# Performance work log

Measured on AMD Instinct MI355X. Metric: run time of the kernel, lower is better.

## Reference

```python
import jax, jax.numpy as jnp
import numpy as np

D_MODEL = 1024
NUM_HEADS = 16
D_K = D_MODEL // NUM_HEADS


def setup_inputs() -> dict:
    key = jax.random.key(0)
    ks = jax.random.split(key, 11)
    B, S = 2, 2048
    scale = 1.0 / np.sqrt(D_MODEL)
    inp = {
        'q': jax.random.normal(ks[0], (B, S, D_MODEL), dtype=jnp.float32),
        'k': jax.random.normal(ks[1], (B, S, D_MODEL), dtype=jnp.float32),
        'v': jax.random.normal(ks[2], (B, S, D_MODEL), dtype=jnp.float32),
        'W_q': jax.random.normal(ks[3], (D_MODEL, D_MODEL), dtype=jnp.float32) * scale,
        'b_q': jnp.zeros((D_MODEL,), dtype=jnp.float32),
        'W_k': jax.random.normal(ks[4], (D_MODEL, D_MODEL), dtype=jnp.float32) * scale,
        'b_k': jnp.zeros((D_MODEL,), dtype=jnp.float32),
        'W_v': jax.random.normal(ks[5], (D_MODEL, D_MODEL), dtype=jnp.float32) * scale,
        'b_v': jnp.zeros((D_MODEL,), dtype=jnp.float32),
        'W_o': jax.random.normal(ks[6], (D_MODEL, D_MODEL), dtype=jnp.float32) * scale,
        'b_o': jnp.zeros((D_MODEL,), dtype=jnp.float32),
    }
    return inp


def _split_heads(x):
    # [B, S, D] -> [B, H, S, d_k]
    B, S, _ = x.shape
    return x.reshape(B, S, NUM_HEADS, D_K).transpose(0, 2, 1, 3)


def reference(q, k, v, W_q, b_q, W_k, b_k, W_v, b_v, W_o, b_o):
    # Linear projections (torch Linear: x @ W.T + b)
    qh = _split_heads(q @ W_q.T + b_q)  # [B,H,S,dk]
    kh = _split_heads(k @ W_k.T + b_k)
    vh = _split_heads(v @ W_v.T + b_v)
    scores = jnp.einsum('bhsd,bhtd->bhst', qh, kh) / jnp.sqrt(
        jnp.asarray(D_K, dtype=qh.dtype))  # [B,H,S,S]
    probs = jax.nn.softmax(scores, axis=-1)
    attn = jnp.einsum('bhst,bhtd->bhsd', probs, vh)  # [B,H,S,dk]
    B, H, S, dk = attn.shape
    combined = attn.transpose(0, 2, 1, 3).reshape(B, S, H * dk)  # [B,S,D]
    return combined @ W_o.T + b_o
```

## Files before the change

### kernel.cpp

```cpp
#include <hip/hip_runtime.h>
#include <hip/hip_bf16.h>

typedef __bf16 bf16;
typedef __attribute__((ext_vector_type(4))) __bf16 bf16x4;
typedef __attribute__((ext_vector_type(8))) __bf16 bf16x8;
typedef __attribute__((ext_vector_type(4))) float f32x4;
typedef __attribute__((ext_vector_type(4))) short short4v;

#define AS1C(p) ((const __attribute__((address_space(1))) void*)(p))
#define AS3(p)  ((__attribute__((address_space(3))) void*)(p))

static constexpr int B_ = 2, S_ = 2048, DM = 1024, H_ = 16, DK = 64;
static constexpr int M_ = B_ * S_;
static constexpr int NW = DM * DM;
static constexpr float QSCL = 0.125f * 1.44269504088896340736f;

__device__ __forceinline__ float fast_exp2(float x) {
#if __has_builtin(__builtin_amdgcn_exp2f)
  return __builtin_amdgcn_exp2f(x);
#else
  return exp2f(x);
#endif
}

__device__ __forceinline__ f32x4 mfma_pv(bf16x4 a, bf16x4 b, f32x4 c) {
#if __has_builtin(__builtin_amdgcn_mfma_f32_16x16x16_bf16)
  return __builtin_amdgcn_mfma_f32_16x16x16_bf16(a, b, c, 0, 0, 0);
#else
  union U { bf16x4 h; short4v s; };
  U ua; ua.h = a;
  U ub; ub.h = b;
  return __builtin_amdgcn_mfma_f32_16x16x16bf16_1k(ua.s, ub.s, c, 0, 0, 0);
#endif
}

__device__ __forceinline__ int vperm_tok(int tok) {
  const int t5 = tok & 31;
  return (tok & ~31) | (((t5 >> 2) & 3) * 8) | (((t5 >> 4) & 1) * 4);
}

__global__ __launch_bounds__(256) void cast_all(
    const float* Wq, const float* Wk, const float* Wv, const float* Wo,
    const float* q, const float* k, const float* v,
    bf16* Wc, bf16* WoC, bf16* qc, bf16* kc, bf16* vc)
{
  const int id = blockIdx.x;
  const float* in;
  bf16* out;
  float s = 1.0f;
  int base;
  if (id < 2048) {
    const int z = id >> 9;
    base = id & 511;
    in  = z == 0 ? Wq : (z == 1 ? Wk : (z == 2 ? Wv : Wo));
    out = z < 3 ? (Wc + (size_t)z * NW) : WoC;
    if (z == 0) s = QSCL;
  } else {
    const int z = (id - 2048) >> 11;
    base = (id - 2048) & 2047;
    in  = z == 0 ? q : (z == 1 ? k : v);
    out = z == 0 ? qc : (z == 1 ? kc : vc);
  }
  const size_t i = ((size_t)base * 256 + threadIdx.x) * 8;
  f32x4 a = *(const f32x4*)(in + i);
  f32x4 b2 = *(const f32x4*)(in + i + 4);
  bf16x8 o;
#pragma unroll
  for (int j = 0; j < 4; ++j) { o[j] = (bf16)(a[j] * s); o[4 + j] = (bf16)(b2[j] * s); }
  *(bf16x8*)(out + i) = o;
}

__global__ __launch_bounds__(256, 3) void gemm_qkv_b(
    const bf16* __restrict__ qc, const bf16* __restrict__ kc,
    const bf16* __restrict__ vc, const bf16* __restrict__ Wc,
    const float* b0, const float* b1, const float* b2,
    bf16* C0, bf16* C1, bf16* C2, int M, int N, int K)
{
  const int id = blockIdx.x;
  const int z  = id >> 8;
  const int r  = id & 255;
  const int by = r & 31;
  const int bx = r >> 5;
  const bf16* A = z == 0 ? qc : (z == 1 ? kc : vc);
  const float* bias = z == 0 ? b0 : (z == 1 ? b1 : b2);
  const float bscale = z == 0 ? QSCL : 1.0f;
  const bf16* W = Wc + (size_t)z * NW;
  bf16* Cout = z == 0 ? C0 : (z == 1 ? C1 : C2);
  const bool transv = (z == 2);

  __shared__ bf16 As[2 * 128 * 32];
  __shared__ bf16 Bs[2 * 128 * 32];

  const int tid  = threadIdx.x;
  const int wave = tid >> 6, lane = tid & 63;
  const int quad = lane >> 4, l16 = lane & 15;
  const int wm = wave >> 1, wn = wave & 1;
  const int row0 = by * 128;
  const int col0 = bx * 128;

  const int srow  = lane >> 2;
  const int skcol = (lane & 3) * 8;

  f32x4 acc[4][4] = {};

  for (int k0 = 0; k0 < K; k0 += 64) {
    __syncthreads();
#pragma unroll
    for (int hf = 0; hf < 2; ++hf)
#pragma unroll
      for (int c = wave; c < 8; c += 4)
        __builtin_amdgcn_global_load_lds(
            AS1C(A + (size_t)(row0 + c * 16 + srow) * K + k0 + hf * 32 + skcol),
            AS3(As + hf * 4096 + c * 512), 16, 0, 0);
#pragma unroll
    for (int hf = 0; hf < 2; ++hf)
#pragma unroll
      for (int i = 0; i < 2; ++i) {
        const int c = wave * 2 + i;
        __builtin_amdgcn_global_load_lds(
            AS1C(W + (size_t)(col0 + c * 16 + srow) * K + k0 + hf * 32 + skcol),
            AS3(Bs + hf * 4096 + c * 512), 16, 0, 0);
      }
    __syncthreads();

#pragma unroll
    for (int hf = 0; hf < 2; ++hf) {
      bf16x8 a[4], bfr[4];
#pragma unroll
      for (int i = 0; i < 4; ++i)
        a[i] = *(const bf16x8*)(As + hf * 4096 + (wm * 64 + i * 16 + l16) * 32 + quad * 8);
#pragma unroll
      for (int j = 0; j < 4; ++j)
        bfr[j] = *(const bf16x8*)(Bs + hf * 4096 + (wn * 64 + j * 16 + l16) * 32 + quad * 8);
#pragma unroll
      for (int i = 0; i < 4; ++i)
#pragma unroll
        for (int j = 0; j < 4; ++j)
          acc[i][j] = __builtin_amdgcn_mfma_f32_16x16x32_bf16(a[i], bfr[j], acc[i][j], 0, 0, 0);
    }
  }

#pragma unroll
  for (int j = 0; j < 4; ++j) {
    const int col = col0 + wn * 64 + j * 16 + l16;
    const float bv = bias[col] * bscale;
    if (transv) {
      const int hh = col >> 6, dd = col & 63;
#pragma unroll
      for (int i = 0; i < 4; ++i) {
        const int row = row0 + wm * 64 + i * 16 + quad * 4;
        const int bb2 = row >> 11, tok = row & 2047;
        const int tokp = vperm_tok(tok);
        bf16x4 o;
#pragma unroll
        for (int r2 = 0; r2 < 4; ++r2) o[r2] = (bf16)(acc[i][j][r2] + bv);
        *(bf16x4*)(Cout + (((size_t)bb2 * H_ + hh) * DK + dd) * S_ + tokp) = o;
      }
    } else {
#pragma unroll
      for (int i = 0; i < 4; ++i)
#pragma unroll
        for (int r2 = 0; r2 < 4; ++r2) {
          const int row = row0 + wm * 64 + i * 16 + quad * 4 + r2;
          Cout[(size_t)row * N + col] = (bf16)(acc[i][j][r2] + bv);
        }
    }
  }
}

__global__ __launch_bounds__(256) void gemm_qkv_f(
    const float* A0, const float* A1, const float* A2,
    const bf16* __restrict__ Wc,
    const float* b0, const float* b1, const float* b2,
    bf16* C0, bf16* C1, bf16* C2, int M, int N, int K)
{
  const int id = blockIdx.x;
  const int z  = id >> 8;
  const int r  = id & 255;
  const int by = r & 31;
  const int bx = r >> 5;
  const float* A = z == 0 ? A0 : (z == 1 ? A1 : A2);
  const float* bias = z == 0 ? b0 : (z == 1 ? b1 : b2);
  const float bscale = z == 0 ? QSCL : 1.0f;
  const bf16* W = Wc + (size_t)z * NW;
  bf16* Cout = z == 0 ? C0 : (z == 1 ? C1 : C2);
  const bool transv = (z == 2);

  __shared__ bf16 As[2 * 128 * 32];
  __shared__ bf16 Bs[2 * 128 * 32];

  const int tid  = threadIdx.x;
  const int wave = tid >> 6, lane = tid & 63;
  const int quad = lane >> 4, l16 = lane & 15;
  const int wm = wave >> 1, wn = wave & 1;
  const int row0 = by * 128;
  const int col0 = bx * 128;

  const int srow  = lane >> 2;
  const int skcol = (lane & 3) * 8;

  const int arow  = (tid >> 1) & 127;
  const int ak16  = (tid & 1) * 16;
  const float* agp = A + (size_t)(row0 + arow) * K + ak16;
  f32x4 pre[8];
#pragma unroll
  for (int hf = 0; hf < 2; ++hf)
#pragma unroll
    for (int c = 0; c < 4; ++c)
      pre[hf * 4 + c] = *(const f32x4*)(agp + hf * 32 + c * 4);

  f32x4 acc[4][4] = {};

  for (int k0 = 0; k0 < K; k0 += 64) {
    __syncthreads();
#pragma unroll
    for (int hf = 0; hf < 2; ++hf) {
      bf16x8 w0, w1;
#pragma unroll
      for (int j = 0; j < 4; ++j) {
        w0[j]     = (bf16)pre[hf * 4 + 0][j];
        w0[4 + j] = (bf16)pre[hf * 4 + 1][j];
        w1[j]     = (bf16)pre[hf * 4 + 2][j];
        w1[4 + j] = (bf16)pre[hf * 4 + 3][j];
      }
      bf16* dst = As + hf * 4096 + arow * 32 + ak16;
      *(bf16x8*)dst = w0;
      *(bf16x8*)(dst + 8) = w1;
    }
#pragma unroll
    for (int hf = 0; hf < 2; ++hf)
#pragma unroll
      for (int i = 0; i < 2; ++i) {
        const int c = wave * 2 + i;
        __builtin_amdgcn_global_load_lds(
            AS1C(W + (size_t)(col0 + c * 16 + srow) * K + k0 + hf * 32 + skcol),
            AS3(Bs + hf * 4096 + c * 512), 16, 0, 0);
      }
    __syncthreads();

    if (k0 + 64 < K) {
#pragma unroll
      for (int hf = 0; hf < 2; ++hf)
#pragma unroll
        for (int c = 0; c < 4; ++c)
          pre[hf * 4 + c] = *(const f32x4*)(agp + k0 + 64 + hf * 32 + c * 4);
    }

#pragma unroll
    for (int hf = 0; hf < 2; ++hf) {
      bf16x8 a[4], bfr[4];
#pragma unroll
      for (int i = 0; i < 4; ++i)
        a[i] = *(const bf16x8*)(As + hf * 4096 + (wm * 64 + i * 16 + l16) * 32 + quad * 8);
#pragma unroll
      for (int j = 0; j < 4; ++j)
        bfr[j] = *(const bf16x8*)(Bs + hf * 4096 + (wn * 64 + j * 16 + l16) * 32 + quad * 8);
#pragma unroll
      for (int i = 0; i < 4; ++i)
#pragma unroll
        for (int j = 0; j < 4; ++j)
          acc[i][j] = __builtin_amdgcn_mfma_f32_16x16x32_bf16(a[i], bfr[j], acc[i][j], 0, 0, 0);
    }
  }

#pragma unroll
  for (int j = 0; j < 4; ++j) {
    const int col = col0 + wn * 64 + j * 16 + l16;
    const float bv = bias[col] * bscale;
    if (transv) {
      const int hh = col >> 6, dd = col & 63;
#pragma unroll
      for (int i = 0; i < 4; ++i) {
        const int row = row0 + wm * 64 + i * 16 + quad * 4;
        const int bb2 = row >> 11, tok = row & 2047;
        const int tokp = vperm_tok(tok);
        bf16x4 o;
#pragma unroll
        for (int r2 = 0; r2 < 4; ++r2) o[r2] = (bf16)(acc[i][j][r2] + bv);
        *(bf16x4*)(Cout + (((size_t)bb2 * H_ + hh) * DK + dd) * S_ + tokp) = o;
      }
    } else {
#pragma unroll
      for (int i = 0; i < 4; ++i)
#pragma unroll
        for (int r2 = 0; r2 < 4; ++r2) {
          const int row = row0 + wm * 64 + i * 16 + quad * 4 + r2;
          Cout[(size_t)row * N + col] = (bf16)(acc[i][j][r2] + bv);
        }
    }
  }
}

__global__ __launch_bounds__(256, 2) void gemm_out(
    const bf16* __restrict__ Ain, const bf16* __restrict__ W,
    const float* __restrict__ bias, float* __restrict__ Cout,
    int M, int N, int K)
{
  const int id = blockIdx.x;
  const int by = id & 63;
  const int bx = id >> 6;

  __shared__ bf16 As0[2 * 64 * 32], As1[2 * 64 * 32];
  __shared__ bf16 Bs0[2 * 128 * 32], Bs1[2 * 128 * 32];

  const int tid  = threadIdx.x;
  const int wave = tid >> 6, lane = tid & 63;
  const int quad = lane >> 4, l16 = lane & 15;
  const int wm = wave >> 1, wn = wave & 1;
  const int row0 = by * 64;
  const int col0 = bx * 128;

  const int srow  = lane >> 2;
  const int skcol = (lane & 3) * 8;

  auto stage_A = [&](int k0, bf16* dst) {
#pragma unroll
    for (int hf = 0; hf < 2; ++hf)
      __builtin_amdgcn_global_load_lds(
          AS1C(Ain + (size_t)(row0 + wave * 16 + srow) * K + k0 + hf * 32 + skcol),
          AS3(dst + hf * 2048 + wave * 512), 16, 0, 0);
  };
  auto stage_W = [&](int k0, bf16* dst) {
#pragma unroll
    for (int hf = 0; hf < 2; ++hf)
#pragma unroll
      for (int i = 0; i < 2; ++i) {
        const int c = wave * 2 + i;
        __builtin_amdgcn_global_load_lds(
            AS1C(W + (size_t)(col0 + c * 16 + srow) * K + k0 + hf * 32 + skcol),
            AS3(dst + hf * 4096 + c * 512), 16, 0, 0);
      }
  };

  f32x4 acc[2][4] = {};

  auto mfma_tile = [&](const bf16* Ab, const bf16* Bb) {
#pragma unroll
    for (int hf = 0; hf < 2; ++hf) {
      bf16x8 a[2], bfr[4];
#pragma unroll
      for (int i = 0; i < 2; ++i)
        a[i] = *(const bf16x8*)(Ab + hf * 2048 + (wm * 32 + i * 16 + l16) * 32 + quad * 8);
#pragma unroll
      for (int j = 0; j < 4; ++j)
        bfr[j] = *(const bf16x8*)(Bb + hf * 4096 + (wn * 64 + j * 16 + l16) * 32 + quad * 8);
#pragma unroll
      for (int i = 0; i < 2; ++i)
#pragma unroll
        for (int j = 0; j < 4; ++j)
          acc[i][j] = __builtin_amdgcn_mfma_f32_16x16x32_bf16(a[i], bfr[j], acc[i][j], 0, 0, 0);
    }
  };

  const int NK = K / 64;
  stage_A(0, As0);
  stage_W(0, Bs0);
  __syncthreads();

  for (int t2 = 0; t2 < NK / 2; ++t2) {
    const int t = t2 * 2;
    if (t + 1 < NK) { stage_A((t + 1) * 64, As1); stage_W((t + 1) * 64, Bs1); }
    mfma_tile(As0, Bs0);
    __syncthreads();
    if (t + 2 < NK) { stage_A((t + 2) * 64, As0); stage_W((t + 2) * 64, Bs0); }
    mfma_tile(As1, Bs1);
    __syncthreads();
  }

#pragma unroll
  for (int j = 0; j < 4; ++j) {
    const int col = col0 + wn * 64 + j * 16 + l16;
    const float bv = bias[col];
#pragma unroll
    for (int i = 0; i < 2; ++i)
#pragma unroll
      for (int r = 0; r < 4; ++r) {
        const int row = row0 + wm * 32 + i * 16 + quad * 4 + r;
        Cout[(size_t)row * N + col] = acc[i][j][r] + bv;
      }
  }
}

__global__ __launch_bounds__(256, 2) void attn_kernel(
    const bf16* Q, const bf16* __restrict__ Kb,
    const bf16* __restrict__ Vtg, bf16* O)
{
  __shared__ bf16 Kt0[64 * 64], Kt1[64 * 64];
  __shared__ bf16 Vt0[64 * 64], Vt1[64 * 64];

  const int tid  = threadIdx.x;
  const int wave = tid >> 6, lane = tid & 63;
  const int quad = lane >> 4, l16 = lane & 15;
  const int id = blockIdx.x;
  const int hb = id & 31;
  const int h = hb & 15, b = hb >> 4;
  const int qt = id >> 5;
  const int qA = qt * 128 + wave * 32;
  const size_t base  = (size_t)b * S_ * DM + (size_t)h * DK;
  const size_t baseV = ((size_t)b * H_ + h) * DK * S_;

  bf16x8 qf[2][2];
#pragma unroll
  for (int f = 0; f < 2; ++f)
#pragma unroll
    for (int kt = 0; kt < 2; ++kt)
      qf[f][kt] = *(const bf16x8*)(Q + base + (size_t)(qA + f * 16 + l16) * DM + kt * 32 + quad * 8);

  const int r8 = lane >> 3;
  const int so = ((lane & 7) ^ r8) << 3;
  const bf16* gK = Kb + base;
  const bf16* gV = Vtg + baseV;

  auto stage = [&](int t, bf16* Kd, bf16* Vd) {
#pragma unroll
    for (int o8 = 0; o8 < 16; o8 += 8) {
      const int row = wave * 16 + o8 + r8;
      __builtin_amdgcn_global_load_lds(
          AS1C(gK + (size_t)(t * 64 + row) * DM + so),
          AS3(Kd + (wave * 16 + o8) * 64), 16, 0, 0);
      __builtin_amdgcn_global_load_lds(
          AS1C(gV + (size_t)row * S_ + t * 64 + so),
          AS3(Vd + (wave * 16 + o8) * 64), 16, 0, 0);
    }
  };

  f32x4 lacc[2] = {};
  f32x4 accO[2][4] = {};
  const int sw = (l16 & 7) << 4;

  auto compute = [&](const bf16* Kc_, const bf16* Vc_) {
    const char* Kc = (const char*)Kc_;
    const char* Vc = (const char*)Vc_;
    f32x4 sc[2][4];
#pragma unroll
    for (int ct = 0; ct < 4; ++ct) {
      const char* kp = Kc + (ct * 16 + l16) * 128;
      const bf16x8 kf0 = *(const bf16x8*)(kp + ((quad * 16) ^ sw));
      const bf16x8 kf1 = *(const bf16x8*)(kp + ((64 + quad * 16) ^ sw));
#pragma unroll
      for (int f = 0; f < 2; ++f) {
        f32x4 a = {0.f, 0.f, 0.f, 0.f};
        a = __builtin_amdgcn_mfma_f32_16x16x32_bf16(kf0, qf[f][0], a, 0, 0, 0);
        a = __builtin_amdgcn_mfma_f32_16x16x32_bf16(kf1, qf[f][1], a, 0, 0, 0);
        sc[f][ct] = a;
      }
    }
    bf16x4 pk[2][4];
#pragma unroll
    for (int f = 0; f < 2; ++f)
#pragma unroll
      for (int ct = 0; ct < 4; ++ct)
#pragma unroll
        for (int r = 0; r < 4; ++r) {
          const float p = fast_exp2(sc[f][ct][r]);
          lacc[f][r] += p;
          pk[f][ct][r] = (bf16)p;
        }
#pragma unroll
    for (int dt = 0; dt < 4; ++dt) {
      const char* vp = Vc + (dt * 16 + l16) * 128;
#pragma unroll
      for (int g = 0; g < 2; ++g) {
        const bf16x8 v8 = *(const bf16x8*)(vp + ((g * 64 + quad * 16) ^ sw));
        const bf16x4 vlo = __builtin_shufflevector(v8, v8, 0, 1, 2, 3);
        const bf16x4 vhi = __builtin_shufflevector(v8, v8, 4, 5, 6, 7);
#pragma unroll
        for (int f = 0; f < 2; ++f) {
          accO[f][dt] = mfma_pv(vlo, pk[f][2 * g],     accO[f][dt]);
          accO[f][dt] = mfma_pv(vhi, pk[f][2 * g + 1], accO[f][dt]);
        }
      }
    }
  };

  constexpr int NIT = S_ / 64;
  stage(0, Kt0, Vt0);
  __syncthreads();

  for (int it = 0; it < NIT; it += 2) {
    if (it + 1 < NIT) stage(it + 1, Kt1, Vt1);
    compute(Kt0, Vt0);
    __syncthreads();
    if (it + 2 < NIT) stage(it + 2, Kt0, Vt0);
    compute(Kt1, Vt1);
    __syncthreads();
  }

#pragma unroll
  for (int f = 0; f < 2; ++f) {
    float l_s = (lacc[f][0] + lacc[f][1]) + (lacc[f][2] + lacc[f][3]);
    l_s += __shfl_xor(l_s, 16, 64);
    l_s += __shfl_xor(l_s, 32, 64);
    const float inv = 1.0f / l_s;
#pragma unroll
    for (int dt = 0; dt < 4; ++dt) {
      bf16x4 o;
#pragma unroll
      for (int r = 0; r < 4; ++r) o[r] = (bf16)(accO[f][dt][r] * inv);
      *(bf16x4*)(O + base + (size_t)(qA + f * 16 + l16) * DM + dt * 16 + quad * 4) = o;
    }
  }
}

extern "C" void kernel_launch(void* const* d_in, const int* in_sizes, int n_in,
                              void* d_out, int out_size, void* d_ws, size_t ws_size,
                              hipStream_t stream) {
  (void)in_sizes; (void)n_in; (void)out_size;
  const float* q  = (const float*)d_in[0];
  const float* k  = (const float*)d_in[1];
  const float* v  = (const float*)d_in[2];
  const float* Wq = (const float*)d_in[3];
  const float* bq = (const float*)d_in[4];
  const float* Wk = (const float*)d_in[5];
  const float* bk = (const float*)d_in[6];
  const float* Wv = (const float*)d_in[7];
  const float* bvv= (const float*)d_in[8];
  const float* Wo = (const float*)d_in[9];
  const float* bo = (const float*)d_in[10];
  float* out = (float*)d_out;

  char* ws = (char*)d_ws;
  const size_t MB = 1024 * 1024;
  bf16* Qb  = (bf16*)(ws);
  bf16* Kbf = (bf16*)(ws + 8 * MB);
  bf16* Vtg = (bf16*)(ws + 16 * MB);
  bf16* Wc  = (bf16*)(ws + 24 * MB);
  bf16* WoC = (bf16*)(ws + 30 * MB);
  bf16* qc  = (bf16*)(ws + 32 * MB);
  bf16* kc  = (bf16*)(ws + 40 * MB);
  bf16* vc  = (bf16*)(ws + 48 * MB);
  bf16* Ab  = Qb;

  const bool big = ws_size >= 60 * MB;
  dim3 bb(256, 1, 1);

  cast_all<<<dim3(big ? 8192 : 2048, 1, 1), bb, 0, stream>>>(
      Wq, Wk, Wv, Wo, q, k, v, Wc, WoC, qc, kc, vc);

  if (big) {
    gemm_qkv_b<<<dim3(768, 1, 1), bb, 0, stream>>>(
        qc, kc, vc, Wc, bq, bk, bvv, Qb, Kbf, Vtg, M_, DM, DM);
  } else {
    gemm_qkv_f<<<dim3(768, 1, 1), bb, 0, stream>>>(
        q, k, v, Wc, bq, bk, bvv, Qb, Kbf, Vtg, M_, DM, DM);
  }

  attn_kernel<<<dim3(512, 1, 1), bb, 0, stream>>>(Qb, Kbf, Vtg, Ab);

  gemm_out<<<dim3(512, 1, 1), bb, 0, stream>>>(Ab, WoC, bo, out, M_, DM, DM);
}
```

Baseline: 214.1 us.

## Software-pipeline attention: overlap next tile's QK^T with current exp and PV

Splits the per-tile attention step into separate QK^T, exp and PV stages, and stages K and V loads separately. K is now prefetched two tiles ahead, and the QK^T MFMAs for tile t+1 are issued before the exp and PV work of tile t. The aim is to give the scheduler independent MFMA and transcendental work to interleave. The cost is a second score buffer held in registers, which raises register pressure and could lower occupancy below the two blocks per SIMD set by launch bounds.

```diff
diff --git a/kernel.cpp b/kernel.cpp
--- a/kernel.cpp
+++ b/kernel.cpp
@@ -385,8 +385,8 @@
     const bf16* Q, const bf16* __restrict__ Kb,
     const bf16* __restrict__ Vtg, bf16* O)
 {
-  __shared__ bf16 Kt0[64 * 64], Kt1[64 * 64];
-  __shared__ bf16 Vt0[64 * 64], Vt1[64 * 64];
+  __shared__ bf16 K0[64 * 64], K1[64 * 64];
+  __shared__ bf16 V0[64 * 64], V1[64 * 64];
 
   const int tid  = threadIdx.x;
   const int wave = tid >> 6, lane = tid & 63;
@@ -411,13 +411,19 @@
   const bf16* gK = Kb + base;
   const bf16* gV = Vtg + baseV;
 
-  auto stage = [&](int t, bf16* Kd, bf16* Vd) {
+  auto stageK = [&](int t, bf16* Kd) {
 #pragma unroll
     for (int o8 = 0; o8 < 16; o8 += 8) {
       const int row = wave * 16 + o8 + r8;
       __builtin_amdgcn_global_load_lds(
           AS1C(gK + (size_t)(t * 64 + row) * DM + so),
           AS3(Kd + (wave * 16 + o8) * 64), 16, 0, 0);
+    }
+  };
+  auto stageV = [&](int t, bf16* Vd) {
+#pragma unroll
+    for (int o8 = 0; o8 < 16; o8 += 8) {
+      const int row = wave * 16 + o8 + r8;
       __builtin_amdgcn_global_load_lds(
           AS1C(gV + (size_t)row * S_ + t * 64 + so),
           AS3(Vd + (wave * 16 + o8) * 64), 16, 0, 0);
@@ -428,10 +434,8 @@
   f32x4 accO[2][4] = {};
   const int sw = (l16 & 7) << 4;
 
-  auto compute = [&](const bf16* Kc_, const bf16* Vc_) {
+  auto qkt = [&](const bf16* Kc_, f32x4 (&sc)[2][4]) {
     const char* Kc = (const char*)Kc_;
-    const char* Vc = (const char*)Vc_;
-    f32x4 sc[2][4];
 #pragma unroll
     for (int ct = 0; ct < 4; ++ct) {
       const char* kp = Kc + (ct * 16 + l16) * 128;
@@ -445,7 +449,9 @@
         sc[f][ct] = a;
       }
     }
-    bf16x4 pk[2][4];
+  };
+
+  auto expv = [&](const f32x4 (&sc)[2][4], bf16x4 (&pk)[2][4]) {
 #pragma unroll
     for (int f = 0; f < 2; ++f)
 #pragma unroll
@@ -456,6 +462,10 @@
           lacc[f][r] += p;
           pk[f][ct][r] = (bf16)p;
         }
+  };
+
+  auto pv = [&](const bf16* Vc_, const bf16x4 (&pk)[2][4]) {
+    const char* Vc = (const char*)Vc_;
 #pragma unroll
     for (int dt = 0; dt < 4; ++dt) {
       const char* vp = Vc + (dt * 16 + l16) * 128;
@@ -474,16 +484,34 @@
   };
 
   constexpr int NIT = S_ / 64;
-  stage(0, Kt0, Vt0);
+  f32x4 scA[2][4], scB[2][4];
+
+  stageK(0, K0);
+  stageK(1, K1);
+  stageV(0, V0);
   __syncthreads();
-
-  for (int it = 0; it < NIT; it += 2) {
-    if (it + 1 < NIT) stage(it + 1, Kt1, Vt1);
-    compute(Kt0, Vt0);
-    __syncthreads();
-    if (it + 2 < NIT) stage(it + 2, Kt0, Vt0);
-    compute(Kt1, Vt1);
-    __syncthreads();
+  qkt(K0, scA);
+  __syncthreads();
+
+  for (int t = 0; t < NIT; t += 2) {
+    {
+      bf16x4 pk[2][4];
+      if (t + 2 < NIT) stageK(t + 2, K0);
+      stageV(t + 1, V1);
+      qkt(K1, scB);
+      expv(scA, pk);
+      pv(V0, pk);
+      __syncthreads();
+    }
+    {
+      bf16x4 pk[2][4];
+      if (t + 3 < NIT) stageK(t + 3, K1);
+      if (t + 2 < NIT) stageV(t + 2, V0);
+      if (t + 2 < NIT) qkt(K0, scA);
+      expv(scB, pk);
+      pv(V1, pk);
+      __syncthreads();
+    }
   }
 
 #pragma unroll
```

Result: no change. 214.6 us (+0.2%).
